# Optimization experiments

Measured on AMD Instinct MI355X. Metric: run time of the kernel, lower is better.

Reference implementation:

```python
import jax, jax.numpy as jnp
import numpy as np

EPS = 1e-12  # F.normalize eps
CLAMP = 30.0
POS_W = 1.0
NEG_W = 1.0
LABEL_SMOOTHING = 0.0


def _l2_normalize(x):
    n = jnp.sqrt(jnp.sum(x * x, axis=-1, keepdims=True))
    return x / jnp.maximum(n, EPS)


def setup_inputs() -> dict:
    key = jax.random.key(0)
    kv, kt = jax.random.split(key)
    B, D = 8192, 512
    video_features = jax.random.normal(kv, (B, D), dtype=jnp.float32)
    text_features = jax.random.normal(kt, (B, D), dtype=jnp.float32)
    log_temp = jnp.asarray(np.log(0.07), dtype=jnp.float32)  # typical CLIP init
    bias = jnp.asarray(-10.0, dtype=jnp.float32)  # bias_init
    return {
        "video_features": video_features,
        "text_features": text_features,
        "log_temp": log_temp,
        "bias": bias,
    }


def reference(video_features, text_features, log_temp, bias):
    v = _l2_normalize(video_features.astype(jnp.float32))  # [B_v, D]
    t = _l2_normalize(text_features.astype(jnp.float32))   # [B_t, D]
    sim = jnp.einsum("vd,td->vt", v, t)                    # [B_v, B_t]
    temp = jnp.exp(log_temp.astype(jnp.float32))
    logits = jnp.clip(sim / temp + bias, -CLAMP, CLAMP)
    B_v, B_t = v.shape[0], t.shape[0]
    m = min(B_v, B_t)
    # diagonal positive labels (pos_mask is None path)
    labels = jnp.zeros((B_v, B_t), jnp.float32).at[jnp.arange(m), jnp.arange(m)].set(1.0)
    if LABEL_SMOOTHING > 0:
        labels = labels * (1 - LABEL_SMOOTHING) + LABEL_SMOOTHING / 2
    weights = jnp.where(labels > 0.5, POS_W, NEG_W).astype(jnp.float32)
    # numerically stable BCE-with-logits, elementwise then weighted mean
    z = logits
    bce = jnp.maximum(z, 0.0) - z * labels + jnp.log1p(jnp.exp(-jnp.abs(z)))
    return jnp.mean(weights * bce)
```

## Files before the change

### kernel.cpp

```cpp
#include <hip/hip_runtime.h>
#include <cstdint>

#define NB 8192
#define ND 512
#define BM 128
#define BN 128
#define BK 64
#define NT (ND / BK)

typedef __bf16 bf16x8 __attribute__((ext_vector_type(8)));
typedef float f32x4 __attribute__((ext_vector_type(4)));

__device__ __forceinline__ unsigned short f2bf(float f) {
    union { float f; uint32_t u; } c; c.f = f;
    return (unsigned short)((c.u + 0x7fffu + ((c.u >> 16) & 1u)) >> 16);
}

__device__ __forceinline__ void load16(const void* g, void* l) {
    __builtin_amdgcn_global_load_lds(
        (void __attribute__((address_space(1)))*)(const_cast<void*>(g)),
        (void __attribute__((address_space(3)))*)(l),
        16, 0, 0);
}

__global__ __launch_bounds__(256) void norm_cast(const float* __restrict__ v,
                                                 const float* __restrict__ t,
                                                 unsigned short* __restrict__ vn,
                                                 unsigned short* __restrict__ tn,
                                                 int ns) {
    const int wave = threadIdx.x >> 6;
    const int lane = threadIdx.x & 63;
    const int row = blockIdx.x * 4 + wave;
    const float* src;
    unsigned short* dst;
    if (row < NB) {
        src = v + (size_t)row * ND;
        dst = vn + (size_t)row * ns;
    } else {
        src = t + (size_t)(row - NB) * ND;
        dst = tn + (size_t)(row - NB) * ns;
    }
    float4 a = ((const float4*)src)[lane * 2];
    float4 b = ((const float4*)src)[lane * 2 + 1];
    float ss = a.x * a.x + a.y * a.y + a.z * a.z + a.w * a.w
             + b.x * b.x + b.y * b.y + b.z * b.z + b.w * b.w;
#pragma unroll
    for (int off = 32; off; off >>= 1) ss += __shfl_xor(ss, off);
    const float sc = 1.0f / fmaxf(sqrtf(ss), 1e-12f);
    union { unsigned short us[8]; uint4 q; } pk;
    pk.us[0] = f2bf(a.x * sc); pk.us[1] = f2bf(a.y * sc);
    pk.us[2] = f2bf(a.z * sc); pk.us[3] = f2bf(a.w * sc);
    pk.us[4] = f2bf(b.x * sc); pk.us[5] = f2bf(b.y * sc);
    pk.us[6] = f2bf(b.z * sc); pk.us[7] = f2bf(b.w * sc);
    ((uint4*)dst)[lane] = pk.q;
}

__global__ __launch_bounds__(256) void gemm_bce(const unsigned short* __restrict__ vn,
                                                const unsigned short* __restrict__ tn,
                                                const float* __restrict__ lt,
                                                const float* __restrict__ bp,
                                                float* __restrict__ out_sum,
                                                int ns) {
    __shared__ __align__(16) unsigned short As[BM * BK];
    __shared__ __align__(16) unsigned short Bs[BN * BK];
    __shared__ float red[4];

    const int tid = threadIdx.x;
    const int lane = tid & 63;
    const int wave = tid >> 6;
    const int wr = wave >> 1;
    const int wc = wave & 1;

    const int m0 = (int)(blockIdx.x >> 6) * BM;
    const int n0 = (int)(blockIdx.x & 63) * BN;

    const int srow = lane >> 3;
    const int schunk = (lane & 7) ^ (srow & 7);
    const unsigned short* ap[4];
    const unsigned short* bq[4];
#pragma unroll
    for (int i = 0; i < 4; ++i) {
        const int rA = m0 + wave * 32 + i * 8 + srow;
        const int rB = n0 + wave * 32 + i * 8 + srow;
        ap[i] = vn + (size_t)rA * ns + schunk * 8;
        bq[i] = tn + (size_t)rB * ns + schunk * 8;
    }

    f32x4 acc[4][4];
#pragma unroll
    for (int i = 0; i < 4; ++i)
#pragma unroll
        for (int j = 0; j < 4; ++j)
            acc[i][j] = f32x4{0.f, 0.f, 0.f, 0.f};

    const int lq = lane & 15;
    const int lh = lane >> 4;
    const int swz0 = lh ^ (lane & 7);

    for (int t = 0; t < NT; ++t) {
        const int k0 = t * BK;
#pragma unroll
        for (int i = 0; i < 4; ++i) {
            load16(ap[i] + k0, As + (wave * 32 + i * 8) * BK);
            load16(bq[i] + k0, Bs + (wave * 32 + i * 8) * BK);
        }
        __syncthreads();

#pragma unroll
        for (int ks = 0; ks < 2; ++ks) {
            const int csw = (swz0 ^ (ks * 4)) * 8;
            bf16x8 af[4], bf[4];
#pragma unroll
            for (int m = 0; m < 4; ++m)
                af[m] = *(const bf16x8*)(As + (wr * 64 + m * 16 + lq) * BK + csw);
#pragma unroll
            for (int n = 0; n < 4; ++n)
                bf[n] = *(const bf16x8*)(Bs + (wc * 64 + n * 16 + lq) * BK + csw);
#pragma unroll
            for (int m = 0; m < 4; ++m)
#pragma unroll
                for (int n = 0; n < 4; ++n)
                    acc[m][n] = __builtin_amdgcn_mfma_f32_16x16x32_bf16(af[m], bf[n], acc[m][n], 0, 0, 0);
        }
        __syncthreads();
    }

    const float invtemp = __expf(-lt[0]);
    const float bias = bp[0];
    float local = 0.f;
    const int row_base = m0 + wr * 64 + lh * 4;
    const int col_base = n0 + wc * 64 + lq;
#pragma unroll
    for (int m = 0; m < 4; ++m) {
#pragma unroll
        for (int n = 0; n < 4; ++n) {
#pragma unroll
            for (int r = 0; r < 4; ++r) {
                const float s = acc[m][n][r];
                float z = fminf(fmaxf(fmaf(s, invtemp, bias), -30.f), 30.f);
                const int gr = row_base + m * 16 + r;
                const int gc = col_base + n * 16;
                float term = fmaxf(z, 0.f) + __logf(1.0f + __expf(-fabsf(z)));
                local += term - ((gr == gc) ? z : 0.f);
            }
        }
    }
#pragma unroll
    for (int off = 32; off; off >>= 1) local += __shfl_xor(local, off);
    if (lane == 0) red[wave] = local;
    __syncthreads();
    if (tid == 0) atomicAdd(out_sum, red[0] + red[1] + red[2] + red[3]);
}

__global__ void finalize_k(float* out) {
    out[0] = out[0] * (1.0f / 67108864.0f);
}

extern "C" void kernel_launch(void* const* d_in, const int* in_sizes, int n_in,
                              void* d_out, int out_size, void* d_ws, size_t ws_size,
                              hipStream_t stream) {
    const float* v = (const float*)d_in[0];
    const float* t = (const float*)d_in[1];
    const float* lt = (const float*)d_in[2];
    const float* bp = (const float*)d_in[3];
    float* out = (float*)d_out;

    const size_t need = (size_t)2 * NB * ND * sizeof(unsigned short);
    unsigned short *vn, *tn;
    int ns;
    if (ws_size >= need) {
        vn = (unsigned short*)d_ws;
        tn = vn + (size_t)NB * ND;
        ns = ND;
    } else {
        vn = (unsigned short*)d_in[0];
        tn = (unsigned short*)d_in[1];
        ns = ND * 2;
    }

    hipMemsetAsync(out, 0, sizeof(float), stream);
    hipLaunchKernelGGL(norm_cast, dim3((2 * NB) / 4), dim3(256), 0, stream, v, t, vn, tn, ns);
    hipLaunchKernelGGL(gemm_bce, dim3((NB / BM) * (NB / BN)), dim3(256), 0, stream,
                       vn, tn, lt, bp, out, ns);
    hipLaunchKernelGGL(finalize_k, dim3(1), dim3(1), 0, stream, out);
}
```

Before: 196.0 us.

## Enlarge GEMM tile to 256x256 with triple-buffered async LDS pipeline

Grows the fused GEMM+BCE block tile to 256x256 with 512 threads and BK=32, and triple-buffers LDS so global-to-LDS loads for step t+2 overlap the MFMA work on step t. A single barrier per k-step uses explicit vmcnt waits, and MFMA issue priority is raised. The separate finalize kernel is removed by folding the mean scaling into each block's atomic add. Larger tiles cut global re-reads and per-block overhead, at the cost of more accumulator registers (128 floats per thread) and lower occupancy.

```diff
diff --git a/kernel.cpp b/kernel.cpp
--- a/kernel.cpp
+++ b/kernel.cpp
@@ -3,10 +3,11 @@
 
 #define NB 8192
 #define ND 512
-#define BM 128
-#define BN 128
-#define BK 64
+#define BM 256
+#define BN 256
+#define BK 32
 #define NT (ND / BK)
+#define THREADS 512
 
 typedef __bf16 bf16x8 __attribute__((ext_vector_type(8)));
 typedef float f32x4 __attribute__((ext_vector_type(4)));
@@ -55,83 +56,101 @@
     ((uint4*)dst)[lane] = pk.q;
 }
 
-__global__ __launch_bounds__(256) void gemm_bce(const unsigned short* __restrict__ vn,
-                                                const unsigned short* __restrict__ tn,
-                                                const float* __restrict__ lt,
-                                                const float* __restrict__ bp,
-                                                float* __restrict__ out_sum,
-                                                int ns) {
-    __shared__ __align__(16) unsigned short As[BM * BK];
-    __shared__ __align__(16) unsigned short Bs[BN * BK];
-    __shared__ float red[4];
+__global__ __launch_bounds__(THREADS) void gemm_bce(const unsigned short* __restrict__ vn,
+                                                    const unsigned short* __restrict__ tn,
+                                                    const float* __restrict__ lt,
+                                                    const float* __restrict__ bp,
+                                                    float* __restrict__ out_sum,
+                                                    int ns) {
+    __shared__ __align__(16) unsigned short smem[3 * 2 * BM * BK];
+    __shared__ float red[8];
 
     const int tid = threadIdx.x;
     const int lane = tid & 63;
     const int wave = tid >> 6;
-    const int wr = wave >> 1;
-    const int wc = wave & 1;
-
-    const int m0 = (int)(blockIdx.x >> 6) * BM;
-    const int n0 = (int)(blockIdx.x & 63) * BN;
-
-    const int srow = lane >> 3;
-    const int schunk = (lane & 7) ^ (srow & 7);
-    const unsigned short* ap[4];
-    const unsigned short* bq[4];
-#pragma unroll
-    for (int i = 0; i < 4; ++i) {
-        const int rA = m0 + wave * 32 + i * 8 + srow;
-        const int rB = n0 + wave * 32 + i * 8 + srow;
-        ap[i] = vn + (size_t)rA * ns + schunk * 8;
-        bq[i] = tn + (size_t)rB * ns + schunk * 8;
-    }
-
-    f32x4 acc[4][4];
-#pragma unroll
-    for (int i = 0; i < 4; ++i)
-#pragma unroll
-        for (int j = 0; j < 4; ++j)
-            acc[i][j] = f32x4{0.f, 0.f, 0.f, 0.f};
-
+    const int wr = wave >> 2;
+    const int wc = wave & 3;
     const int lq = lane & 15;
     const int lh = lane >> 4;
-    const int swz0 = lh ^ (lane & 7);
-
+
+    const int m0 = (int)(blockIdx.x >> 5) * BM;
+    const int n0 = (int)(blockIdx.x & 31) * BN;
+
+    const int srow = tid >> 2;
+    const int schunk = (tid & 3) ^ (srow & 3);
+    const unsigned short* a0 = vn + (size_t)(m0 + srow) * ns + schunk * 8;
+    const unsigned short* a1 = vn + (size_t)(m0 + 128 + srow) * ns + schunk * 8;
+    const unsigned short* b0 = tn + (size_t)(n0 + srow) * ns + schunk * 8;
+    const unsigned short* b1 = tn + (size_t)(n0 + 128 + srow) * ns + schunk * 8;
+
+#define STAGE(t, b) do {                                                   \
+        const int k0_ = (t) * BK;                                          \
+        unsigned short* As_ = smem + (b) * (2 * BM * BK);                  \
+        unsigned short* Bs_ = As_ + BM * BK;                               \
+        load16(a0 + k0_, As_ + wave * 512);                                \
+        load16(a1 + k0_, As_ + 4096 + wave * 512);                         \
+        load16(b0 + k0_, Bs_ + wave * 512);                                \
+        load16(b1 + k0_, Bs_ + 4096 + wave * 512);                         \
+    } while (0)
+
+    const int swz = (lh ^ (lq & 3)) * 8;
+    const int aoff = (wr * 128 + lq) * BK + swz;
+    const int boff = (wc * 64 + lq) * BK + swz;
+
+    f32x4 acc[8][4];
+#pragma unroll
+    for (int m = 0; m < 8; ++m)
+#pragma unroll
+        for (int n = 0; n < 4; ++n)
+            acc[m][n] = f32x4{0.f, 0.f, 0.f, 0.f};
+
+    STAGE(0, 0);
+    STAGE(1, 1);
+    asm volatile("s_waitcnt vmcnt(4)" ::: "memory");
+    __builtin_amdgcn_s_barrier();
+    __builtin_amdgcn_sched_barrier(0);
+
+#pragma unroll
     for (int t = 0; t < NT; ++t) {
-        const int k0 = t * BK;
-#pragma unroll
-        for (int i = 0; i < 4; ++i) {
-            load16(ap[i] + k0, As + (wave * 32 + i * 8) * BK);
-            load16(bq[i] + k0, Bs + (wave * 32 + i * 8) * BK);
+        const unsigned short* As_ = smem + (t % 3) * (2 * BM * BK);
+        const unsigned short* Bs_ = As_ + BM * BK;
+        bf16x8 af[8], bfr[4];
+#pragma unroll
+        for (int m = 0; m < 8; ++m)
+            af[m] = *(const bf16x8*)(As_ + aoff + m * 512);
+#pragma unroll
+        for (int n = 0; n < 4; ++n)
+            bfr[n] = *(const bf16x8*)(Bs_ + boff + n * 512);
+
+        if (t + 2 < NT) STAGE(t + 2, (t + 2) % 3);
+
+        __builtin_amdgcn_s_setprio(1);
+#pragma unroll
+        for (int m = 0; m < 8; ++m)
+#pragma unroll
+            for (int n = 0; n < 4; ++n)
+                acc[m][n] = __builtin_amdgcn_mfma_f32_16x16x32_bf16(af[m], bfr[n], acc[m][n], 0, 0, 0);
+        __builtin_amdgcn_s_setprio(0);
+
+        if (t < NT - 2) {
+            asm volatile("s_waitcnt vmcnt(4)" ::: "memory");
+            __builtin_amdgcn_s_barrier();
+            __builtin_amdgcn_sched_barrier(0);
+        } else if (t == NT - 2) {
+            asm volatile("s_waitcnt vmcnt(0)" ::: "memory");
+            __builtin_amdgcn_s_barrier();
+            __builtin_amdgcn_sched_barrier(0);
         }
-        __syncthreads();
-
-#pragma unroll
-        for (int ks = 0; ks < 2; ++ks) {
-            const int csw = (swz0 ^ (ks * 4)) * 8;
-            bf16x8 af[4], bf[4];
-#pragma unroll
-            for (int m = 0; m < 4; ++m)
-                af[m] = *(const bf16x8*)(As + (wr * 64 + m * 16 + lq) * BK + csw);
-#pragma unroll
-            for (int n = 0; n < 4; ++n)
-                bf[n] = *(const bf16x8*)(Bs + (wc * 64 + n * 16 + lq) * BK + csw);
-#pragma unroll
-            for (int m = 0; m < 4; ++m)
-#pragma unroll
-                for (int n = 0; n < 4; ++n)
-                    acc[m][n] = __builtin_amdgcn_mfma_f32_16x16x32_bf16(af[m], bf[n], acc[m][n], 0, 0, 0);
-        }
-        __syncthreads();
-    }
+    }
+#undef STAGE
 
     const float invtemp = __expf(-lt[0]);
     const float bias = bp[0];
     float local = 0.f;
-    const int row_base = m0 + wr * 64 + lh * 4;
+    const int row_base = m0 + wr * 128 + lh * 4;
     const int col_base = n0 + wc * 64 + lq;
 #pragma unroll
-    for (int m = 0; m < 4; ++m) {
+    for (int m = 0; m < 8; ++m) {
 #pragma unroll
         for (int n = 0; n < 4; ++n) {
 #pragma unroll
@@ -140,8 +159,7 @@
                 float z = fminf(fmaxf(fmaf(s, invtemp, bias), -30.f), 30.f);
                 const int gr = row_base + m * 16 + r;
                 const int gc = col_base + n * 16;
-                float term = fmaxf(z, 0.f) + __logf(1.0f + __expf(-fabsf(z)));
-                local += term - ((gr == gc) ? z : 0.f);
+                local += fmaxf(z, 0.f) + __logf(1.0f + __expf(-fabsf(z))) - ((gr == gc) ? z : 0.f);
             }
         }
     }
@@ -149,11 +167,12 @@
     for (int off = 32; off; off >>= 1) local += __shfl_xor(local, off);
     if (lane == 0) red[wave] = local;
     __syncthreads();
-    if (tid == 0) atomicAdd(out_sum, red[0] + red[1] + red[2] + red[3]);
-}
-
-__global__ void finalize_k(float* out) {
-    out[0] = out[0] * (1.0f / 67108864.0f);
+    if (tid == 0) {
+        float tot = 0.f;
+#pragma unroll
+        for (int w = 0; w < 8; ++w) tot += red[w];
+        atomicAdd(out_sum, tot * (1.0f / 67108864.0f));
+    }
 }
 
 extern "C" void kernel_launch(void* const* d_in, const int* in_sizes, int n_in,
@@ -180,7 +199,6 @@
 
     hipMemsetAsync(out, 0, sizeof(float), stream);
     hipLaunchKernelGGL(norm_cast, dim3((2 * NB) / 4), dim3(256), 0, stream, v, t, vn, tn, ns);
-    hipLaunchKernelGGL(gemm_bce, dim3((NB / BM) * (NB / BN)), dim3(256), 0, stream,
+    hipLaunchKernelGGL(gemm_bce, dim3((NB / BM) * (NB / BN)), dim3(THREADS), 0, stream,
                        vn, tn, lt, bp, out, ns);
-    hipLaunchKernelGGL(finalize_k, dim3(1), dim3(1), 0, stream, out);
-}
+}
```

Result: faster. 179.7 us (-8.3%).
